# Kernel optimization log

Measured on AMD Instinct MI355X. Metric: run time of the kernel, lower is better.

Reference implementation:

```python
import jax, jax.numpy as jnp
import numpy as np

B, T, I, H, D = 256, 256, 64, 512, 256  # batch, seq_len, input_size, lstm_units, dense_units
R_ON = 0.05    # time-gate open ratio
ALPHA = 1e-3   # leak during closed phase
LN_EPS = 1e-5


def setup_inputs() -> dict:
    key = jax.random.key(0)
    ks = jax.random.split(key, 12)
    sc_in = 1.0 / np.sqrt(I)
    sc_h = 1.0 / np.sqrt(H)
    return {
        "x":  jax.random.normal(ks[0], (B, T, I), dtype=jnp.float32),
        # PLSTM weights (4 gates: i, f, g, o)
        "W":  jax.random.uniform(ks[1], (I, 4 * H), minval=-sc_in, maxval=sc_in, dtype=jnp.float32),
        "U":  jax.random.uniform(ks[2], (H, 4 * H), minval=-sc_h, maxval=sc_h, dtype=jnp.float32),
        "b":  jnp.zeros((4 * H,), dtype=jnp.float32),
        # Phased-LSTM time-gate parameters (per hidden unit)
        "tau": jnp.exp(jax.random.uniform(ks[3], (H,), minval=0.0, maxval=3.0, dtype=jnp.float32)),
        "s":   jax.random.uniform(ks[4], (H,), minval=0.0, maxval=10.0, dtype=jnp.float32),
        # LayerNorm
        "ln_gamma": jnp.ones((H,), dtype=jnp.float32),
        "ln_beta":  jnp.zeros((H,), dtype=jnp.float32),
        # Dense head
        "W1": jax.random.uniform(ks[5], (H, D), minval=-sc_h, maxval=sc_h, dtype=jnp.float32),
        "b1": jnp.zeros((D,), dtype=jnp.float32),
        "W2": jax.random.uniform(ks[6], (D, 1), minval=-1.0 / np.sqrt(D), maxval=1.0 / np.sqrt(D), dtype=jnp.float32),
        "b2": jnp.zeros((1,), dtype=jnp.float32),
    }


def _plstm_last_h(x, W, U, b, tau, s):
    # x: [B, T, I] -> last hidden state [B, H] of the phased LSTM
    xT = jnp.swapaxes(x, 0, 1)                 # [T, B, I]
    times = jnp.arange(x.shape[1], dtype=x.dtype)  # timestamps 0..T-1

    def step(carry, inp):
        h, c = carry
        x_t, t = inp
        z = x_t @ W + h @ U + b                # [B, 4H]
        i_g, f_g, g_g, o_g = jnp.split(z, 4, axis=-1)
        c_tilde = jax.nn.sigmoid(f_g) * c + jax.nn.sigmoid(i_g) * jnp.tanh(g_g)
        h_tilde = jax.nn.sigmoid(o_g) * jnp.tanh(c_tilde)
        # time gate k(t): piecewise-linear oscillation, per hidden unit
        phi = jnp.mod(t - s, tau) / tau        # [H]
        k = jnp.where(phi < 0.5 * R_ON, 2.0 * phi / R_ON,
             jnp.where(phi < R_ON, 2.0 - 2.0 * phi / R_ON, ALPHA * phi))
        c_new = k * c_tilde + (1.0 - k) * c
        h_new = k * h_tilde + (1.0 - k) * h
        return (h_new, c_new), None

    h0 = jnp.zeros((x.shape[0], tau.shape[0]), dtype=x.dtype)
    (h_last, _), _ = jax.lax.scan(step, (h0, h0), (xT, times))
    return h_last


def reference(x, W, U, b, tau, s, ln_gamma, ln_beta, W1, b1, W2, b2):
    h = _plstm_last_h(x, W, U, b, tau, s)      # [B, H] (== out[:, -1, :])
    # LayerNorm over hidden dim (per-position, so applying to last step is exact)
    mu = jnp.mean(h, axis=-1, keepdims=True)
    var = jnp.var(h, axis=-1, keepdims=True)
    hn = (h - mu) * jax.lax.rsqrt(var + LN_EPS) * ln_gamma + ln_beta
    # dropout layers are identity in eval mode
    out = hn @ W1 + b1
    out = out @ W2 + b2                        # [B, 1]
    return out
```

## Files before the change

kernel.cpp:

```cpp
#include <hip/hip_runtime.h>
#include <cmath>

#define NB 256
#define NT 512
#define NG 16
#define GB 16
#define B_ 256
#define T_ 256
#define I_ 64
#define H_ 512
#define G4H 2048
#define BT 16
#define UT 32
#define ZP 132
#define NFC 18
#define CPQ 17
#define CSTR 68
#define NCELL 1224
#define HPS_STR 36
#define R_ON_F 0.05f
#define ALPHA_F 1.0e-3f
#define LN_EPS_F 1.0e-5f

typedef _Float16 h8 __attribute__((ext_vector_type(8)));
typedef _Float16 h4v __attribute__((ext_vector_type(4)));
typedef float f4 __attribute__((ext_vector_type(4)));
typedef float v4f __attribute__((ext_vector_type(4)));

__device__ __align__(16) float g_h[2][B_ * H_];

struct alignas(256) PadCnt { unsigned v; unsigned pad[63]; };
__device__ PadCnt g_cnt2[NG];
__device__ PadCnt g_gen2[NG];
__device__ PadCnt g_flag[NG][GB];

__device__ __forceinline__ float fast_sigmoid(float x) {
    return __builtin_amdgcn_rcpf(1.f + __expf(-x));
}
__device__ __forceinline__ float fast_tanh(float x) {
    return 1.f - 2.f * __builtin_amdgcn_rcpf(__expf(2.f * x) + 1.f);
}

struct HiLo { _Float16 hi, lo; };
__device__ __forceinline__ HiLo cvt_hilo(float v) {
    HiLo r;
    r.hi = (_Float16)v;
    r.lo = (_Float16)(v - (float)r.hi);
    return r;
}

__global__ __launch_bounds__(NT, 1) void plstm_scan_kernel(
    const float* __restrict__ x, const float* __restrict__ W,
    const float* __restrict__ U, const float* __restrict__ bias,
    const float* __restrict__ tau, const float* __restrict__ sph,
    const float* __restrict__ ln_g, const float* __restrict__ ln_b,
    const float* __restrict__ W1, const float* __restrict__ b1,
    const float* __restrict__ W2, const float* __restrict__ b2,
    float* __restrict__ out)
{
    __shared__ __align__(16) _Float16 Ah[NCELL * 8];
    __shared__ __align__(16) float zs[BT][ZP];
    __shared__ __align__(16) float hps[BT * HPS_STR];
    __shared__ __align__(16) float bsz[128];
    __shared__ float red[16];

    const int tid = threadIdx.x;
    const int bt = blockIdx.x >> 4;
    const int ut = blockIdx.x & 15;
    const int b0 = bt * BT;
    const int u0 = ut * UT;

    if (tid == 0) {
        unsigned z = 0;
        asm volatile("global_store_dword %0, %1, off sc0 sc1\n\ts_waitcnt vmcnt(0)"
                     :: "v"(&g_flag[bt][ut].v), "v"(z) : "memory");
    }

    const int wv = tid >> 6;
    const int lane = tid & 63;
    const int n_ = lane & 15;
    const int q_ = lane >> 4;

    const int jg = (wv >> 1) * 512 + u0 + (wv & 1) * 16 + n_;
    h8 Bh[NFC], Bl[NFC];
    #pragma unroll
    for (int c = 0; c < NFC; ++c) {
        #pragma unroll
        for (int e = 0; e < 8; ++e) {
            const int kk = c * 32 + q_ * 8 + e;
            float v;
            if (c < 2) v = W[(size_t)kk * G4H + jg];
            else       v = U[(size_t)(kk - I_) * G4H + jg];
            const HiLo hl = cvt_hilo(v);
            Bh[c][e] = hl.hi;
            Bl[c][e] = hl.lo;
        }
    }
    if (tid < 128) bsz[tid] = bias[((tid >> 5) << 9) + u0 + (tid & 31)];

    const int urow = tid >> 5;
    const int uu   = tid & 31;
    const float tau_r = tau[u0 + uu];
    const float s_r   = sph[u0 + uu];
    float c_st = 0.f;

    const int xr = (tid >> 4) & 15, xc4 = (tid & 15) << 2;
    const int cX = (tid & 15) >> 3, qX = ((tid & 15) >> 1) & 3;
    const int e0 = (tid & 1) << 2;
    const int fX = (cX * CSTR + qX * CPQ + xr) * 8 + e0;
    const int hr0 = tid >> 7, hk4 = (tid & 127) << 2;
    const int cS = 2 + ((tid & 127) >> 3), qS = ((tid & 127) >> 1) & 3;
    const int srcblk = (tid & 127) >> 3;
    const int mloc = (tid & 127) - (u0 >> 2);
    const bool own = (mloc >= 0) && (mloc < 8);
    const int dof = mloc << 2;

    float4 xv = *(const float4*)(x + ((size_t)(b0 + xr) * T_ + 0) * I_ + xc4);

    const int fb = (q_ * CPQ + n_) * 8;

    int cur = 0;
    for (int t = 0; t < T_; ++t) {
        if (t == 0) {
            const h8 z8 = {};
            for (int idx = tid; idx < NCELL; idx += NT)
                *(h8*)&Ah[idx * 8] = z8;
            if (tid < (BT * HPS_STR) / 4) {
                const v4f zf = {0.f, 0.f, 0.f, 0.f};
                *(v4f*)&hps[tid * 4] = zf;
            }
            __syncthreads();
            if (tid < 256) {
                h4v xh;
                xh[0] = (_Float16)xv.x; xh[1] = (_Float16)xv.y;
                xh[2] = (_Float16)xv.z; xh[3] = (_Float16)xv.w;
                *(h4v*)&Ah[fX] = xh;
            }
        } else {
            if (t >= 2) {
                const unsigned want = (unsigned)t;
                const unsigned* fp = &g_flag[bt][srcblk].v;
                unsigned v;
                do {
                    asm volatile("global_load_dword %0, %1, off sc0 sc1\n\ts_waitcnt vmcnt(0)"
                                 : "=v"(v) : "v"(fp) : "memory");
                } while (__ballot(v < want));
            }
            const float* hb = g_h[cur] + (size_t)(b0 + hr0) * H_ + hk4;
            v4f a0, a1, a2, a3;
            asm volatile(
                "global_load_dwordx4 %0, %4, off sc0 sc1\n\t"
                "global_load_dwordx4 %1, %5, off sc0 sc1\n\t"
                "global_load_dwordx4 %2, %6, off sc0 sc1\n\t"
                "global_load_dwordx4 %3, %7, off sc0 sc1"
                : "=&v"(a0), "=&v"(a1), "=&v"(a2), "=&v"(a3)
                : "v"(hb), "v"(hb + 4 * H_), "v"(hb + 8 * H_), "v"(hb + 12 * H_)
                : "memory");
            asm volatile("s_waitcnt vmcnt(0)"
                : "+v"(a0), "+v"(a1), "+v"(a2), "+v"(a3) :: "memory");
            const v4f av[4] = {a0, a1, a2, a3};
            #pragma unroll
            for (int it = 0; it < 4; ++it) {
                const int row = hr0 + 4 * it;
                const int fidx = (cS * CSTR + qS * CPQ + row) * 8 + e0;
                h4v hh;
                hh[0] = (_Float16)av[it][0]; hh[1] = (_Float16)av[it][1];
                hh[2] = (_Float16)av[it][2]; hh[3] = (_Float16)av[it][3];
                *(h4v*)&Ah[fidx] = hh;
                if (own) *(v4f*)&hps[row * HPS_STR + dof] = av[it];
            }
        }
        __syncthreads();

        if (tid < 256) {
            const int tn = (t < T_ - 1) ? t + 1 : t;
            xv = *(const float4*)(x + ((size_t)(b0 + xr) * T_ + tn) * I_ + xc4);
        }

        f4 ac0 = {0.f, 0.f, 0.f, 0.f};
        f4 ac1 = {0.f, 0.f, 0.f, 0.f};
        #pragma unroll
        for (int c = 0; c < NFC; ++c) {
            const h8 ah = *(const h8*)&Ah[fb + c * (CSTR * 8)];
            ac0 = __builtin_amdgcn_mfma_f32_16x16x32_f16(ah, Bh[c], ac0, 0, 0, 0);
            ac1 = __builtin_amdgcn_mfma_f32_16x16x32_f16(ah, Bl[c], ac1, 0, 0, 0);
        }
        const f4 zt = ac0 + ac1;
        {
            const int colz = wv * 16 + n_;
            const int rz = q_ * 4;
            zs[rz + 0][colz] = zt[0];
            zs[rz + 1][colz] = zt[1];
            zs[rz + 2][colz] = zt[2];
            zs[rz + 3][colz] = zt[3];
        }
        __syncthreads();

        {
            const float zi = zs[urow][uu]       + bsz[uu];
            const float zf = zs[urow][32 + uu]  + bsz[32 + uu];
            const float zg = zs[urow][64 + uu]  + bsz[64 + uu];
            const float zo = zs[urow][96 + uu]  + bsz[96 + uu];
            const float si = fast_sigmoid(zi);
            const float sf = fast_sigmoid(zf);
            const float so = fast_sigmoid(zo);
            const float ct = sf * c_st + si * fast_tanh(zg);
            const float ht = so * fast_tanh(ct);
            float aa = (float)t - s_r;
            float rr = fmodf(aa, tau_r);
            if (rr < 0.f) rr += tau_r;
            const float phi = rr / tau_r;
            float kk;
            if (phi < 0.5f * R_ON_F)      kk = phi * (2.f / R_ON_F);
            else if (phi < R_ON_F)        kk = 2.f - phi * (2.f / R_ON_F);
            else                          kk = ALPHA_F * phi;
            const float hprev = hps[urow * HPS_STR + uu];
            const float hn = kk * ht + (1.f - kk) * hprev;
            c_st = kk * ct + (1.f - kk) * c_st;
            float* gp = g_h[cur ^ 1] + (size_t)(b0 + urow) * H_ + (u0 + uu);
            asm volatile("global_store_dword %0, %1, off sc0 sc1\n\ts_waitcnt vmcnt(0)"
                         :: "v"(gp), "v"(hn) : "memory");
        }
        __syncthreads();

        if (tid == 0) {
            unsigned fv = (unsigned)(t + 1);
            asm volatile("global_store_dword %0, %1, off sc0 sc1"
                         :: "v"(&g_flag[bt][ut].v), "v"(fv) : "memory");
        }
        if (t < T_ - 1 && tid < 256) {
            h4v xh;
            xh[0] = (_Float16)xv.x; xh[1] = (_Float16)xv.y;
            xh[2] = (_Float16)xv.z; xh[3] = (_Float16)xv.w;
            *(h4v*)&Ah[fX] = xh;
        }
        if (t == 0) {
            if (tid == 0) {
                unsigned gen = __hip_atomic_load(&g_gen2[bt].v, __ATOMIC_RELAXED, __HIP_MEMORY_SCOPE_SYSTEM);
                unsigned a = __hip_atomic_fetch_add(&g_cnt2[bt].v, 1u, __ATOMIC_RELAXED, __HIP_MEMORY_SCOPE_SYSTEM);
                if (a == GB - 1u) {
                    __hip_atomic_store(&g_cnt2[bt].v, 0u, __ATOMIC_RELAXED, __HIP_MEMORY_SCOPE_SYSTEM);
                    asm volatile("s_waitcnt vmcnt(0)" ::: "memory");
                    __hip_atomic_store(&g_gen2[bt].v, gen + 1u, __ATOMIC_RELAXED, __HIP_MEMORY_SCOPE_SYSTEM);
                } else {
                    while (__hip_atomic_load(&g_gen2[bt].v, __ATOMIC_RELAXED, __HIP_MEMORY_SCOPE_SYSTEM) == gen)
                        __builtin_amdgcn_s_sleep(1);
                }
            }
            __syncthreads();
        }
        cur ^= 1;
    }

    {
        if (tid < 64) {
            const unsigned want = (unsigned)T_;
            const unsigned* fp = &g_flag[bt][tid & 15].v;
            unsigned v;
            do {
                asm volatile("global_load_dword %0, %1, off sc0 sc1\n\ts_waitcnt vmcnt(0)"
                             : "=v"(v) : "v"(fp) : "memory");
            } while (__ballot(v < want));
        }
        __syncthreads();

        const int b = blockIdx.x;
        float hv;
        const float* hp = g_h[cur] + (size_t)b * H_ + tid;
        asm volatile("global_load_dword %0, %1, off sc0 sc1\n\ts_waitcnt vmcnt(0)"
                     : "=v"(hv) : "v"(hp) : "memory");
        float s1 = hv, s2 = hv * hv;
        #pragma unroll
        for (int off = 32; off > 0; off >>= 1) {
            s1 += __shfl_down(s1, off, 64);
            s2 += __shfl_down(s2, off, 64);
        }
        const int ln = tid & 63;
        if (ln == 0) { red[wv] = s1; red[8 + wv] = s2; }
        __syncthreads();
        float S1 = 0.f, S2 = 0.f;
        #pragma unroll
        for (int w = 0; w < 8; ++w) { S1 += red[w]; S2 += red[8 + w]; }
        const float mu = S1 * (1.f / 512.f);
        const float var = S2 * (1.f / 512.f) - mu * mu;
        const float rstd = rsqrtf(var + LN_EPS_F);
        const float hn = (hv - mu) * rstd * ln_g[tid] + ln_b[tid];
        float w12 = 0.f;
        const float* w1p = W1 + (size_t)tid * 256;
        #pragma unroll 4
        for (int d = 0; d < 256; ++d) w12 = fmaf(w1p[d], W2[d], w12);
        float contrib = hn * w12;
        if (tid < 256) contrib = fmaf(b1[tid], W2[tid], contrib);
        #pragma unroll
        for (int off = 32; off > 0; off >>= 1) contrib += __shfl_down(contrib, off, 64);
        __syncthreads();
        if (ln == 0) red[wv] = contrib;
        __syncthreads();
        if (tid == 0) {
            float tot = b2[0];
            #pragma unroll
            for (int w = 0; w < 8; ++w) tot += red[w];
            out[b] = tot;
        }
    }
}

extern "C" void kernel_launch(void* const* d_in, const int* in_sizes, int n_in,
                              void* d_out, int out_size, void* d_ws, size_t ws_size,
                              hipStream_t stream) {
    const float* x   = (const float*)d_in[0];
    const float* W   = (const float*)d_in[1];
    const float* U   = (const float*)d_in[2];
    const float* b   = (const float*)d_in[3];
    const float* tau = (const float*)d_in[4];
    const float* s   = (const float*)d_in[5];
    const float* lng = (const float*)d_in[6];
    const float* lnb = (const float*)d_in[7];
    const float* W1  = (const float*)d_in[8];
    const float* b1  = (const float*)d_in[9];
    const float* W2  = (const float*)d_in[10];
    const float* b2  = (const float*)d_in[11];
    float* out = (float*)d_out;
    plstm_scan_kernel<<<dim3(NB), dim3(NT), 0, stream>>>(
        x, W, U, b, tau, s, lng, lnb, W1, b1, W2, b2, out);
}
```

Measured before the change: 890.2 us.

## Pack fp16 hidden state with step tag to replace per-step flag barrier

Each hidden value is now written as a 32-bit word holding the fp16 value in the high half and the step index in the low half. Consumers spin on the data loads themselves until every tag matches, so the separate flag polling, the extra __syncthreads and the flag store are gone from each step. The previous own-unit h is kept in a register instead of being reloaded from shared memory. The final step writes fp32 h to a separate buffer for the LayerNorm head. The cost is that tag checks have to be done on every loaded word, and a 16-bit tag that only works because T is small.

```diff
diff --git a/kernel.cpp b/kernel.cpp
--- a/kernel.cpp
+++ b/kernel.cpp
@@ -17,7 +17,6 @@
 #define CPQ 17
 #define CSTR 68
 #define NCELL 1224
-#define HPS_STR 36
 #define R_ON_F 0.05f
 #define ALPHA_F 1.0e-3f
 #define LN_EPS_F 1.0e-5f
@@ -26,8 +25,11 @@
 typedef _Float16 h4v __attribute__((ext_vector_type(4)));
 typedef float f4 __attribute__((ext_vector_type(4)));
 typedef float v4f __attribute__((ext_vector_type(4)));
-
-__device__ __align__(16) float g_h[2][B_ * H_];
+typedef unsigned u4 __attribute__((ext_vector_type(4)));
+typedef unsigned short us4 __attribute__((ext_vector_type(4)));
+
+__device__ __align__(16) unsigned g_hp[2][B_ * H_];
+__device__ __align__(16) float g_hf[B_ * H_];
 
 struct alignas(256) PadCnt { unsigned v; unsigned pad[63]; };
 __device__ PadCnt g_cnt2[NG];
@@ -60,7 +62,6 @@
 {
     __shared__ __align__(16) _Float16 Ah[NCELL * 8];
     __shared__ __align__(16) float zs[BT][ZP];
-    __shared__ __align__(16) float hps[BT * HPS_STR];
     __shared__ __align__(16) float bsz[128];
     __shared__ float red[16];
 
@@ -70,10 +71,21 @@
     const int b0 = bt * BT;
     const int u0 = ut * UT;
 
+    const int urow = tid >> 5;
+    const int uu   = tid & 31;
+
     if (tid == 0) {
         unsigned z = 0;
         asm volatile("global_store_dword %0, %1, off sc0 sc1\n\ts_waitcnt vmcnt(0)"
                      :: "v"(&g_flag[bt][ut].v), "v"(z) : "memory");
+    }
+    {
+        const size_t slot = (size_t)(b0 + urow) * H_ + (u0 + uu);
+        unsigned z = 0;
+        asm volatile("global_store_dword %0, %2, off sc0 sc1\n\t"
+                     "global_store_dword %1, %2, off sc0 sc1\n\t"
+                     "s_waitcnt vmcnt(0)"
+                     :: "v"(&g_hp[0][slot]), "v"(&g_hp[1][slot]), "v"(z) : "memory");
     }
 
     const int wv = tid >> 6;
@@ -98,11 +110,10 @@
     }
     if (tid < 128) bsz[tid] = bias[((tid >> 5) << 9) + u0 + (tid & 31)];
 
-    const int urow = tid >> 5;
-    const int uu   = tid & 31;
     const float tau_r = tau[u0 + uu];
     const float s_r   = sph[u0 + uu];
     float c_st = 0.f;
+    float h_st = 0.f;
 
     const int xr = (tid >> 4) & 15, xc4 = (tid & 15) << 2;
     const int cX = (tid & 15) >> 3, qX = ((tid & 15) >> 1) & 3;
@@ -110,10 +121,6 @@
     const int fX = (cX * CSTR + qX * CPQ + xr) * 8 + e0;
     const int hr0 = tid >> 7, hk4 = (tid & 127) << 2;
     const int cS = 2 + ((tid & 127) >> 3), qS = ((tid & 127) >> 1) & 3;
-    const int srcblk = (tid & 127) >> 3;
-    const int mloc = (tid & 127) - (u0 >> 2);
-    const bool own = (mloc >= 0) && (mloc < 8);
-    const int dof = mloc << 2;
 
     float4 xv = *(const float4*)(x + ((size_t)(b0 + xr) * T_ + 0) * I_ + xc4);
 
@@ -125,10 +132,6 @@
             const h8 z8 = {};
             for (int idx = tid; idx < NCELL; idx += NT)
                 *(h8*)&Ah[idx * 8] = z8;
-            if (tid < (BT * HPS_STR) / 4) {
-                const v4f zf = {0.f, 0.f, 0.f, 0.f};
-                *(v4f*)&hps[tid * 4] = zf;
-            }
             __syncthreads();
             if (tid < 256) {
                 h4v xh;
@@ -137,37 +140,40 @@
                 *(h4v*)&Ah[fX] = xh;
             }
         } else {
-            if (t >= 2) {
-                const unsigned want = (unsigned)t;
-                const unsigned* fp = &g_flag[bt][srcblk].v;
-                unsigned v;
-                do {
-                    asm volatile("global_load_dword %0, %1, off sc0 sc1\n\ts_waitcnt vmcnt(0)"
-                                 : "=v"(v) : "v"(fp) : "memory");
-                } while (__ballot(v < want));
-            }
-            const float* hb = g_h[cur] + (size_t)(b0 + hr0) * H_ + hk4;
-            v4f a0, a1, a2, a3;
-            asm volatile(
-                "global_load_dwordx4 %0, %4, off sc0 sc1\n\t"
-                "global_load_dwordx4 %1, %5, off sc0 sc1\n\t"
-                "global_load_dwordx4 %2, %6, off sc0 sc1\n\t"
-                "global_load_dwordx4 %3, %7, off sc0 sc1"
-                : "=&v"(a0), "=&v"(a1), "=&v"(a2), "=&v"(a3)
-                : "v"(hb), "v"(hb + 4 * H_), "v"(hb + 8 * H_), "v"(hb + 12 * H_)
-                : "memory");
-            asm volatile("s_waitcnt vmcnt(0)"
-                : "+v"(a0), "+v"(a1), "+v"(a2), "+v"(a3) :: "memory");
-            const v4f av[4] = {a0, a1, a2, a3};
+            const unsigned* hb = g_hp[cur] + (size_t)(b0 + hr0) * H_ + hk4;
+            const unsigned want = (unsigned)t;
+            u4 a0, a1, a2, a3;
+            bool ok;
+            do {
+                asm volatile(
+                    "global_load_dwordx4 %0, %4, off sc0 sc1\n\t"
+                    "global_load_dwordx4 %1, %5, off sc0 sc1\n\t"
+                    "global_load_dwordx4 %2, %6, off sc0 sc1\n\t"
+                    "global_load_dwordx4 %3, %7, off sc0 sc1\n\t"
+                    "s_waitcnt vmcnt(0)"
+                    : "=&v"(a0), "=&v"(a1), "=&v"(a2), "=&v"(a3)
+                    : "v"(hb), "v"(hb + 4 * H_), "v"(hb + 8 * H_), "v"(hb + 12 * H_)
+                    : "memory");
+                ok = ((a0[0] & 0xFFFFu) == want) & ((a0[1] & 0xFFFFu) == want)
+                   & ((a0[2] & 0xFFFFu) == want) & ((a0[3] & 0xFFFFu) == want)
+                   & ((a1[0] & 0xFFFFu) == want) & ((a1[1] & 0xFFFFu) == want)
+                   & ((a1[2] & 0xFFFFu) == want) & ((a1[3] & 0xFFFFu) == want)
+                   & ((a2[0] & 0xFFFFu) == want) & ((a2[1] & 0xFFFFu) == want)
+                   & ((a2[2] & 0xFFFFu) == want) & ((a2[3] & 0xFFFFu) == want)
+                   & ((a3[0] & 0xFFFFu) == want) & ((a3[1] & 0xFFFFu) == want)
+                   & ((a3[2] & 0xFFFFu) == want) & ((a3[3] & 0xFFFFu) == want);
+            } while (__ballot(!ok));
+            const u4 av[4] = {a0, a1, a2, a3};
             #pragma unroll
             for (int it = 0; it < 4; ++it) {
                 const int row = hr0 + 4 * it;
                 const int fidx = (cS * CSTR + qS * CPQ + row) * 8 + e0;
-                h4v hh;
-                hh[0] = (_Float16)av[it][0]; hh[1] = (_Float16)av[it][1];
-                hh[2] = (_Float16)av[it][2]; hh[3] = (_Float16)av[it][3];
-                *(h4v*)&Ah[fidx] = hh;
-                if (own) *(v4f*)&hps[row * HPS_STR + dof] = av[it];
+                us4 uv;
+                uv[0] = (unsigned short)(av[it][0] >> 16);
+                uv[1] = (unsigned short)(av[it][1] >> 16);
+                uv[2] = (unsigned short)(av[it][2] >> 16);
+                uv[3] = (unsigned short)(av[it][3] >> 16);
+                *(us4*)&Ah[fidx] = uv;
             }
         }
         __syncthreads();
@@ -214,20 +220,31 @@
             if (phi < 0.5f * R_ON_F)      kk = phi * (2.f / R_ON_F);
             else if (phi < R_ON_F)        kk = 2.f - phi * (2.f / R_ON_F);
             else                          kk = ALPHA_F * phi;
-            const float hprev = hps[urow * HPS_STR + uu];
-            const float hn = kk * ht + (1.f - kk) * hprev;
+            const float hn = kk * ht + (1.f - kk) * h_st;
             c_st = kk * ct + (1.f - kk) * c_st;
-            float* gp = g_h[cur ^ 1] + (size_t)(b0 + urow) * H_ + (u0 + uu);
-            asm volatile("global_store_dword %0, %1, off sc0 sc1\n\ts_waitcnt vmcnt(0)"
-                         :: "v"(gp), "v"(hn) : "memory");
-        }
-        __syncthreads();
-
-        if (tid == 0) {
-            unsigned fv = (unsigned)(t + 1);
-            asm volatile("global_store_dword %0, %1, off sc0 sc1"
-                         :: "v"(&g_flag[bt][ut].v), "v"(fv) : "memory");
-        }
+            h_st = hn;
+            if (t < T_ - 1) {
+                const unsigned short hb16 = __builtin_bit_cast(unsigned short, (_Float16)hn);
+                const unsigned packed = ((unsigned)hb16 << 16) | (unsigned)(t + 1);
+                unsigned* gp = g_hp[cur ^ 1] + (size_t)(b0 + urow) * H_ + (u0 + uu);
+                asm volatile("global_store_dword %0, %1, off sc0 sc1"
+                             :: "v"(gp), "v"(packed) : "memory");
+            } else {
+                float* gp = g_hf + (size_t)(b0 + urow) * H_ + (u0 + uu);
+                asm volatile("global_store_dword %0, %1, off sc0 sc1\n\ts_waitcnt vmcnt(0)"
+                             :: "v"(gp), "v"(hn) : "memory");
+            }
+        }
+
+        if (t == T_ - 1) {
+            __syncthreads();
+            if (tid == 0) {
+                unsigned fv = (unsigned)T_;
+                asm volatile("global_store_dword %0, %1, off sc0 sc1"
+                             :: "v"(&g_flag[bt][ut].v), "v"(fv) : "memory");
+            }
+        }
+
         if (t < T_ - 1 && tid < 256) {
             h4v xh;
             xh[0] = (_Float16)xv.x; xh[1] = (_Float16)xv.y;
@@ -266,7 +283,7 @@
 
         const int b = blockIdx.x;
         float hv;
-        const float* hp = g_h[cur] + (size_t)b * H_ + tid;
+        const float* hp = g_hf + (size_t)b * H_ + tid;
         asm volatile("global_load_dword %0, %1, off sc0 sc1\n\ts_waitcnt vmcnt(0)"
                      : "=v"(hv) : "v"(hp) : "memory");
         float s1 = hv, s2 = hv * hv;
```

New measurement: 791.5 us. 11.1% less time.
